# Kernel tuning notes

Hardware: AMD Instinct MI355X
Metric: run time of the kernel (lower is better)

The kernel has to match this reference:

```python
import jax, jax.numpy as jnp
import numpy as np

EMB = 1024
HEADS = 16
HEAD_DIM = EMB // HEADS
SEQ = 2048
BATCH = 2
FF = 4 * EMB


def gelu_tanh(x):
    # matches the hand-rolled GELU: 0.5*x*(1+tanh(sqrt(2/pi)*(x+0.044715*x^3)))
    c = jnp.sqrt(jnp.asarray(2.0 / jnp.pi, dtype=x.dtype))
    return 0.5 * x * (1.0 + jnp.tanh(c * (x + 0.044715 * x ** 3)))


def layernorm(x, scale, shift, eps=1e-5):
    mean = jnp.mean(x, axis=-1, keepdims=True)
    var = jnp.var(x, axis=-1, keepdims=True)  # unbiased=False
    return scale * (x - mean) * jax.lax.rsqrt(var + eps) + shift


def setup_inputs() -> dict:
    key = jax.random.key(0)
    ks = jax.random.split(key, 10)
    s = 1.0 / np.sqrt(EMB)
    sf = 1.0 / np.sqrt(FF)
    return {
        "x": jax.random.normal(ks[0], (BATCH, SEQ, EMB), jnp.float32),
        "Wq": jax.random.uniform(ks[1], (EMB, EMB), jnp.float32, -s, s),
        "Wk": jax.random.uniform(ks[2], (EMB, EMB), jnp.float32, -s, s),
        "Wv": jax.random.uniform(ks[3], (EMB, EMB), jnp.float32, -s, s),
        "Wo": jax.random.uniform(ks[4], (EMB, EMB), jnp.float32, -s, s),
        "bo": jnp.zeros((EMB,), jnp.float32),
        "ln1_g": jnp.ones((EMB,), jnp.float32),
        "ln1_b": jnp.zeros((EMB,), jnp.float32),
        "ln2_g": jnp.ones((EMB,), jnp.float32),
        "ln2_b": jnp.zeros((EMB,), jnp.float32),
        "W1": jax.random.uniform(ks[5], (EMB, FF), jnp.float32, -s, s),
        "b1": jnp.zeros((FF,), jnp.float32),
        "W2": jax.random.uniform(ks[6], (FF, EMB), jnp.float32, -sf, sf),
        "b2": jnp.zeros((EMB,), jnp.float32),
    }


def reference(x, Wq, Wk, Wv, Wo, bo, ln1_g, ln1_b, ln2_g, ln2_b, W1, b1, W2, b2):
    b, n, d = x.shape
    shortcut = x
    h = layernorm(x, ln1_g, ln1_b)
    # projections -> [b, heads, n, head_dim]
    def split_heads(t):
        return t.reshape(b, n, HEADS, HEAD_DIM).transpose(0, 2, 1, 3)
    q = split_heads(h @ Wq)
    k = split_heads(h @ Wk)
    v = split_heads(h @ Wv)
    scores = jnp.einsum("bhqd,bhkd->bhqk", q, k)
    causal = jnp.triu(jnp.ones((n, n), dtype=bool), k=1)
    scores = jnp.where(causal, -jnp.inf, scores)
    weights = jax.nn.softmax(scores / jnp.sqrt(jnp.asarray(HEAD_DIM, x.dtype)), axis=-1)
    ctx = jnp.einsum("bhqk,bhkd->bhqd", weights, v)
    ctx = ctx.transpose(0, 2, 1, 3).reshape(b, n, d)
    attn_out = ctx @ Wo + bo
    x = attn_out + shortcut
    shortcut = x
    h = layernorm(x, ln2_g, ln2_b)
    ff = gelu_tanh(h @ W1 + b1) @ W2 + b2
    return ff + shortcut
```

## Files before the change

kernel.cpp:

```cpp
#include <hip/hip_runtime.h>

typedef __bf16 bf16x8 __attribute__((ext_vector_type(8)));
typedef float f32x4 __attribute__((ext_vector_type(4)));
typedef unsigned short u16;

#define EMB 1024
#define SEQ 2048
#define BATCH 2
#define HEADS 16
#define HEAD_DIM 64
#define FF 4096
#define ROWS (BATCH * SEQ)

static __device__ __forceinline__ u16 f2bf(float f) {
    unsigned int u = __builtin_bit_cast(unsigned int, f);
    unsigned int r = (u + 0x7FFFu + ((u >> 16) & 1u)) >> 16;
    return (u16)r;
}

static __device__ __forceinline__ unsigned int pack_bf_trunc(float a, float b) {
    return __builtin_amdgcn_perm(__builtin_bit_cast(unsigned int, a),
                                 __builtin_bit_cast(unsigned int, b), 0x07060302u);
}

static __device__ __forceinline__ void gload16(const u16* g, u16* l) {
    __builtin_amdgcn_global_load_lds(
        (const __attribute__((address_space(1))) unsigned int*)(const void*)g,
        (__attribute__((address_space(3))) unsigned int*)(void*)l, 16, 0, 0);
}

__global__ __launch_bounds__(256) void transpose_f32_to_bf16(
    const float* __restrict__ in, u16* __restrict__ out, int R, int C) {
    __shared__ float tile[32][33];
    int c0 = blockIdx.x * 32, r0 = blockIdx.y * 32;
    int tx = threadIdx.x & 31, ty = threadIdx.x >> 5;
#pragma unroll
    for (int i = 0; i < 32; i += 8)
        tile[ty + i][tx] = in[(size_t)(r0 + ty + i) * C + c0 + tx];
    __syncthreads();
#pragma unroll
    for (int i = 0; i < 32; i += 8)
        out[(size_t)(c0 + ty + i) * R + r0 + tx] = f2bf(tile[tx][ty + i]);
}

__global__ __launch_bounds__(256) void transpose4_f32_to_bf16(
    const float* __restrict__ s0, const float* __restrict__ s1,
    const float* __restrict__ s2, const float* __restrict__ s3,
    u16* __restrict__ d0, u16* __restrict__ d1,
    u16* __restrict__ d2, u16* __restrict__ d3) {
    __shared__ float tile[32][33];
    const float* in;
    u16* out;
    switch (blockIdx.z) {
        case 0: in = s0; out = d0; break;
        case 1: in = s1; out = d1; break;
        case 2: in = s2; out = d2; break;
        default: in = s3; out = d3; break;
    }
    int c0 = blockIdx.x * 32, r0 = blockIdx.y * 32;
    int tx = threadIdx.x & 31, ty = threadIdx.x >> 5;
#pragma unroll
    for (int i = 0; i < 32; i += 8)
        tile[ty + i][tx] = in[(size_t)(r0 + ty + i) * EMB + c0 + tx];
    __syncthreads();
#pragma unroll
    for (int i = 0; i < 32; i += 8)
        out[(size_t)(c0 + ty + i) * EMB + r0 + tx] = f2bf(tile[tx][ty + i]);
}

__global__ __launch_bounds__(256) void ln_kernel(
    const float* __restrict__ x, const float* __restrict__ gamma,
    const float* __restrict__ beta, u16* __restrict__ out) {
    int row = blockIdx.x;
    int t = threadIdx.x;
    float4 v = reinterpret_cast<const float4*>(x + (size_t)row * EMB)[t];
    float s = v.x + v.y + v.z + v.w;
    float s2 = v.x * v.x + v.y * v.y + v.z * v.z + v.w * v.w;
#pragma unroll
    for (int off = 1; off < 64; off <<= 1) {
        s += __shfl_xor(s, off);
        s2 += __shfl_xor(s2, off);
    }
    __shared__ float sm[8];
    int wid = t >> 6;
    if ((t & 63) == 0) { sm[wid] = s; sm[wid + 4] = s2; }
    __syncthreads();
    s = sm[0] + sm[1] + sm[2] + sm[3];
    s2 = sm[4] + sm[5] + sm[6] + sm[7];
    float mean = s * (1.0f / EMB);
    float var = s2 * (1.0f / EMB) - mean * mean;
    float inv = rsqrtf(var + 1e-5f);
    float4 gv = reinterpret_cast<const float4*>(gamma)[t];
    float4 bv = reinterpret_cast<const float4*>(beta)[t];
    ushort4 o;
    o.x = f2bf((v.x - mean) * inv * gv.x + bv.x);
    o.y = f2bf((v.y - mean) * inv * gv.y + bv.y);
    o.z = f2bf((v.z - mean) * inv * gv.z + bv.z);
    o.w = f2bf((v.w - mean) * inv * gv.w + bv.w);
    reinterpret_cast<ushort4*>(out + (size_t)row * EMB)[t] = o;
}

template <int EPI, int BN>
__global__ __launch_bounds__(256) void gemm_bf16(
    const u16* __restrict__ A, const u16* __restrict__ B, void* __restrict__ Cout,
    const float* __restrict__ bias, const float* __restrict__ resid,
    void* __restrict__ Cout2, void* __restrict__ Cout3,
    int M, int N, int K) {
    __shared__ u16 As[128 * 64];
    __shared__ u16 Bs[BN * 64];
    constexpr int MI = (BN == 128) ? 4 : 2;
    constexpr int BSW = BN / 32;
    int tm = blockIdx.x * 128;
    int tn = blockIdx.y * BN;
    int t = threadIdx.x;
    int lane = t & 63, wid = t >> 6;
    int wr, wc;
    if constexpr (BN == 128) { wr = (wid >> 1) * 64; wc = (wid & 1) * 64; }
    else { wr = wid * 32; wc = 0; }
    int l15 = lane & 15, g = lane >> 4;
    const u16* Abase = A + (size_t)tm * K;
    const u16* Bbase = B + (size_t)tn * K;
    f32x4 acc[MI][4] = {};
    for (int k0 = 0; k0 < K; k0 += 64) {
        __syncthreads();
#pragma unroll
        for (int p = 0; p < 4; ++p) {
            int chunk = (wid * 4 + p) * 64 + lane;
            int row = chunk >> 3, c8 = (chunk & 7) * 8;
            gload16(Abase + (size_t)row * K + k0 + c8, &As[(wid * 4 + p) * 512]);
        }
#pragma unroll
        for (int p = 0; p < BSW; ++p) {
            int chunk = (wid * BSW + p) * 64 + lane;
            int row = chunk >> 3, c8 = (chunk & 7) * 8;
            gload16(Bbase + (size_t)row * K + k0 + c8, &Bs[(wid * BSW + p) * 512]);
        }
        __syncthreads();
#pragma unroll
        for (int kc = 0; kc < 2; ++kc) {
            int ko = kc * 32 + g * 8;
            bf16x8 af[MI], bfr[4];
#pragma unroll
            for (int i = 0; i < MI; ++i)
                af[i] = *reinterpret_cast<const bf16x8*>(&As[(wr + i * 16 + l15) * 64 + ko]);
#pragma unroll
            for (int j = 0; j < 4; ++j)
                bfr[j] = *reinterpret_cast<const bf16x8*>(&Bs[(wc + j * 16 + l15) * 64 + ko]);
#pragma unroll
            for (int i = 0; i < MI; ++i)
#pragma unroll
                for (int j = 0; j < 4; ++j)
                    acc[i][j] = __builtin_amdgcn_mfma_f32_16x16x32_bf16(af[i], bfr[j], acc[i][j], 0, 0, 0);
        }
    }
    int mb = tm + wr + g * 4;
    int nb = tn + wc + l15;
#pragma unroll
    for (int i = 0; i < MI; ++i) {
#pragma unroll
        for (int j = 0; j < 4; ++j) {
            int n = nb + j * 16;
#pragma unroll
            for (int r = 0; r < 4; ++r) {
                int m = mb + i * 16 + r;
                float val = acc[i][j][r];
                if constexpr (EPI == 0) {
                    ((u16*)Cout)[(size_t)m * N + n] = f2bf(val);
                } else if constexpr (EPI == 1) {
                    ((float*)Cout)[(size_t)m * N + n] =
                        val + bias[n] + resid[(size_t)m * N + n];
                } else if constexpr (EPI == 2) {
                    float xg = val + bias[n];
                    float x3 = xg + 0.044715f * xg * xg * xg;
                    float tz = 0.7978845608028654f * x3;
                    float th = 1.0f - 2.0f / (1.0f + __expf(2.0f * tz));
                    ((u16*)Cout)[(size_t)m * N + n] = f2bf(0.5f * xg * (1.0f + th));
                } else {
                    if (n < 1024) {
                        ((u16*)Cout)[(size_t)m * 1024 + n] = f2bf(val);
                    } else if (n < 2048) {
                        ((u16*)Cout2)[(size_t)m * 1024 + (n - 1024)] = f2bf(val);
                    } else {
                        int bb = m >> 11, ss = m & 2047;
                        ((u16*)Cout3)[((size_t)(bb * EMB + (n - 2048))) * SEQ + ss] = f2bf(val);
                    }
                }
            }
        }
    }
}

__global__ __launch_bounds__(64) void attn_kernel(
    const u16* __restrict__ Qb, const u16* __restrict__ Kb,
    const u16* __restrict__ Vt, u16* __restrict__ ctx) {
    __shared__ u16 P_lds[32][72];
    int bh = blockIdx.x;
    int b = bh >> 4, h = bh & 15;
    int qc = 63 - (int)blockIdx.y;
    int lane = threadIdx.x;
    int l15 = lane & 15, g = lane >> 4;
    int qbase = qc * 32;

    const u16* Qrow = Qb + (size_t)(b * SEQ) * EMB + h * 64;
    const u16* Krow = Kb + (size_t)(b * SEQ) * EMB + h * 64;
    const u16* Vrow = Vt + (size_t)(b * EMB + h * 64) * SEQ;

    bf16x8 qf[2][2];
#pragma unroll
    for (int qt = 0; qt < 2; ++qt)
#pragma unroll
        for (int kc = 0; kc < 2; ++kc) {
            bf16x8 v = *reinterpret_cast<const bf16x8*>(
                Qrow + (size_t)(qbase + qt * 16 + l15) * EMB + kc * 32 + g * 8);
            bf16x8 sv;
#pragma unroll
            for (int e = 0; e < 8; ++e) sv[e] = (__bf16)((float)v[e] * 0.125f);
            qf[qt][kc] = sv;
        }

    f32x4 ctx_acc[2][4] = {};
    float mrun[2] = {-1e30f, -1e30f};
    float lrun[2] = {0.f, 0.f};
    int nkt = qc / 2 + 1;

    bf16x8 kcur[8], knxt[8];
#pragma unroll
    for (int i = 0; i < 8; ++i) {
        int kc = i >> 2, ktile = i & 3;
        kcur[i] = *reinterpret_cast<const bf16x8*>(
            Krow + (size_t)(ktile * 16 + l15) * EMB + kc * 32 + g * 8);
    }

    for (int kt = 0; kt < nkt; ++kt) {
        int k0 = kt * 64;
        bool last = (kt == nkt - 1);
        bf16x8 vf[8];
#pragma unroll
        for (int i = 0; i < 8; ++i) {
            int kc = i >> 2, dt = i & 3;
            vf[i] = *reinterpret_cast<const bf16x8*>(
                Vrow + (size_t)(dt * 16 + l15) * SEQ + k0 + kc * 32 + g * 8);
        }
        f32x4 sacc[4][2] = {};
#pragma unroll
        for (int kc = 0; kc < 2; ++kc)
#pragma unroll
            for (int ktile = 0; ktile < 4; ++ktile)
#pragma unroll
                for (int qt = 0; qt < 2; ++qt)
                    sacc[ktile][qt] = __builtin_amdgcn_mfma_f32_16x16x32_bf16(
                        kcur[kc * 4 + ktile], qf[qt][kc], sacc[ktile][qt], 0, 0, 0);
        if (kt + 1 < nkt) {
#pragma unroll
            for (int i = 0; i < 8; ++i) {
                int kc = i >> 2, ktile = i & 3;
                knxt[i] = *reinterpret_cast<const bf16x8*>(
                    Krow + (size_t)(k0 + 64 + ktile * 16 + l15) * EMB + kc * 32 + g * 8);
            }
        }
#pragma unroll
        for (int qt = 0; qt < 2; ++qt) {
            float sv[16];
            float tmax = -1e30f;
            if (last) {
                int q = qbase + qt * 16 + l15;
#pragma unroll
                for (int ktile = 0; ktile < 4; ++ktile)
#pragma unroll
                    for (int r = 0; r < 4; ++r) {
                        int key = k0 + ktile * 16 + g * 4 + r;
                        float sx = (key > q) ? -1e30f : sacc[ktile][qt][r];
                        sv[ktile * 4 + r] = sx;
                        tmax = fmaxf(tmax, sx);
                    }
            } else {
#pragma unroll
                for (int ktile = 0; ktile < 4; ++ktile)
#pragma unroll
                    for (int r = 0; r < 4; ++r) {
                        float sx = sacc[ktile][qt][r];
                        sv[ktile * 4 + r] = sx;
                        tmax = fmaxf(tmax, sx);
                    }
            }
            tmax = fmaxf(tmax, __shfl_xor(tmax, 16));
            tmax = fmaxf(tmax, __shfl_xor(tmax, 32));
            if (!__all(tmax <= mrun[qt] + 8.0f)) {
                float mnew = fmaxf(mrun[qt], tmax);
                float corr = __expf(mrun[qt] - mnew);
                mrun[qt] = mnew;
                lrun[qt] *= corr;
                float corr4[4];
#pragma unroll
                for (int r = 0; r < 4; ++r) corr4[r] = __shfl(corr, g * 4 + r);
#pragma unroll
                for (int dt = 0; dt < 4; ++dt)
#pragma unroll
                    for (int r = 0; r < 4; ++r) ctx_acc[qt][dt][r] *= corr4[r];
            }
            float m = mrun[qt];
            float psum = 0.f;
#pragma unroll
            for (int idx = 0; idx < 16; ++idx) {
                float p = __expf(sv[idx] - m);
                sv[idx] = p;
                psum += p;
            }
            lrun[qt] += psum;
#pragma unroll
            for (int ktile = 0; ktile < 4; ++ktile) {
                uint2 w;
                w.x = pack_bf_trunc(sv[ktile * 4 + 1], sv[ktile * 4 + 0]);
                w.y = pack_bf_trunc(sv[ktile * 4 + 3], sv[ktile * 4 + 2]);
                *reinterpret_cast<uint2*>(&P_lds[qt * 16 + l15][ktile * 16 + g * 4]) = w;
            }
        }
        asm volatile("s_waitcnt lgkmcnt(0)" ::: "memory");
#pragma unroll
        for (int kc = 0; kc < 2; ++kc) {
            bf16x8 pf[2];
#pragma unroll
            for (int qt = 0; qt < 2; ++qt)
                pf[qt] = *reinterpret_cast<const bf16x8*>(&P_lds[qt * 16 + l15][kc * 32 + g * 8]);
#pragma unroll
            for (int dt = 0; dt < 4; ++dt)
#pragma unroll
                for (int qt = 0; qt < 2; ++qt)
                    ctx_acc[qt][dt] = __builtin_amdgcn_mfma_f32_16x16x32_bf16(
                        pf[qt], vf[kc * 4 + dt], ctx_acc[qt][dt], 0, 0, 0);
        }
#pragma unroll
        for (int i = 0; i < 8; ++i) kcur[i] = knxt[i];
    }
#pragma unroll
    for (int qt = 0; qt < 2; ++qt) {
        float lsum = lrun[qt];
        lsum += __shfl_xor(lsum, 16);
        lsum += __shfl_xor(lsum, 32);
        float d4[4];
#pragma unroll
        for (int r = 0; r < 4; ++r) d4[r] = __shfl(lsum, g * 4 + r);
#pragma unroll
        for (int dt = 0; dt < 4; ++dt)
#pragma unroll
            for (int r = 0; r < 4; ++r) {
                int q = qbase + qt * 16 + g * 4 + r;
                int d = h * 64 + dt * 16 + l15;
                ctx[(size_t)(b * SEQ + q) * EMB + d] = f2bf(ctx_acc[qt][dt][r] / d4[r]);
            }
    }
}

extern "C" void kernel_launch(void* const* d_in, const int* in_sizes, int n_in,
                              void* d_out, int out_size, void* d_ws, size_t ws_size,
                              hipStream_t stream) {
    const float* x    = (const float*)d_in[0];
    const float* Wq   = (const float*)d_in[1];
    const float* Wk   = (const float*)d_in[2];
    const float* Wv   = (const float*)d_in[3];
    const float* Wo   = (const float*)d_in[4];
    const float* bo   = (const float*)d_in[5];
    const float* ln1g = (const float*)d_in[6];
    const float* ln1b = (const float*)d_in[7];
    const float* ln2g = (const float*)d_in[8];
    const float* ln2b = (const float*)d_in[9];
    const float* W1   = (const float*)d_in[10];
    const float* b1   = (const float*)d_in[11];
    const float* W2   = (const float*)d_in[12];
    const float* b2   = (const float*)d_in[13];

    char* ws = (char*)d_ws;
    size_t off = 0;
    auto alloc = [&](size_t bytes) {
        void* p = ws + off;
        off += (bytes + 255) & ~(size_t)255;
        return p;
    };
    u16* h1     = (u16*)alloc((size_t)ROWS * EMB * 2);
    u16* Wqkvt  = (u16*)alloc((size_t)3 * EMB * EMB * 2);
    u16* Wot    = (u16*)alloc((size_t)EMB * EMB * 2);
    u16* W1t    = (u16*)alloc((size_t)FF * EMB * 2);
    u16* W2t    = (u16*)alloc((size_t)EMB * FF * 2);
    u16* Qb     = (u16*)alloc((size_t)ROWS * EMB * 2);
    u16* Kb     = (u16*)alloc((size_t)ROWS * EMB * 2);
    u16* Vtb    = (u16*)alloc((size_t)BATCH * EMB * SEQ * 2);
    u16* ctxb   = (u16*)alloc((size_t)ROWS * EMB * 2);
    float* x2   = (float*)alloc((size_t)ROWS * EMB * 4);
    u16* h2     = (u16*)alloc((size_t)ROWS * EMB * 2);
    u16* ff1    = (u16*)alloc((size_t)ROWS * FF * 2);

    u16* Wqt = Wqkvt;
    u16* Wkt = Wqkvt + (size_t)EMB * EMB;
    u16* Wvt = Wqkvt + (size_t)2 * EMB * EMB;

    transpose4_f32_to_bf16<<<dim3(32, 32, 4), 256, 0, stream>>>(
        Wq, Wk, Wv, Wo, Wqt, Wkt, Wvt, Wot);
    transpose_f32_to_bf16<<<dim3(128, 32), 256, 0, stream>>>(W1, W1t, EMB, FF);
    transpose_f32_to_bf16<<<dim3(32, 128), 256, 0, stream>>>(W2, W2t, FF, EMB);

    ln_kernel<<<ROWS, 256, 0, stream>>>(x, ln1g, ln1b, h1);

    gemm_bf16<4, 128><<<dim3(32, 24), 256, 0, stream>>>(h1, Wqkvt, Qb, nullptr, nullptr,
                                                        Kb, Vtb, ROWS, 3072, EMB);

    attn_kernel<<<dim3(32, 64), 64, 0, stream>>>(Qb, Kb, Vtb, ctxb);

    gemm_bf16<1, 64><<<dim3(32, 16), 256, 0, stream>>>(ctxb, Wot, x2, bo, x,
                                                       nullptr, nullptr, ROWS, EMB, EMB);

    ln_kernel<<<ROWS, 256, 0, stream>>>(x2, ln2g, ln2b, h2);

    gemm_bf16<2, 128><<<dim3(32, 32), 256, 0, stream>>>(h2, W1t, ff1, b1, nullptr,
                                                        nullptr, nullptr, ROWS, FF, EMB);
    gemm_bf16<1, 64><<<dim3(32, 16), 256, 0, stream>>>(ff1, W2t, (float*)d_out, b2, x2,
                                                       nullptr, nullptr, ROWS, EMB, FF);
}
```

Measured before the change: 415.2 us.

## Switch attention to 32x32x16 MFMA with register-resident P via permlane32 swap

Rewrites the attention kernel to use 32x32x16 bf16 MFMAs over one 32-query tile. The P matrix now stays in registers, rearranged with v_permlane32_swap instead of a round-trip through LDS. The softmax scale and log2(e) are folded into the Q projection epilogue so the kernel can use exp2 and skip per-load Q scaling. The K double-buffer is dropped and launch bounds request 2 waves per EU. This cuts LDS traffic, shuffles and instruction count, at the risk of higher register pressure and load latency no longer being hidden by the prefetch buffer.

```diff
diff --git a/kernel.cpp b/kernel.cpp
--- a/kernel.cpp
+++ b/kernel.cpp
@@ -2,6 +2,8 @@
 
 typedef __bf16 bf16x8 __attribute__((ext_vector_type(8)));
 typedef float f32x4 __attribute__((ext_vector_type(4)));
+typedef float f32x16 __attribute__((ext_vector_type(16)));
+typedef unsigned int u32x4 __attribute__((ext_vector_type(4)));
 typedef unsigned short u16;
 
 #define EMB 1024
@@ -11,6 +13,8 @@
 #define HEAD_DIM 64
 #define FF 4096
 #define ROWS (BATCH * SEQ)
+
+#define QSCALE 0.18033688011112042f
 
 static __device__ __forceinline__ u16 f2bf(float f) {
     unsigned int u = __builtin_bit_cast(unsigned int, f);
@@ -177,7 +181,7 @@
                     ((u16*)Cout)[(size_t)m * N + n] = f2bf(0.5f * xg * (1.0f + th));
                 } else {
                     if (n < 1024) {
-                        ((u16*)Cout)[(size_t)m * 1024 + n] = f2bf(val);
+                        ((u16*)Cout)[(size_t)m * 1024 + n] = f2bf(val * QSCALE);
                     } else if (n < 2048) {
                         ((u16*)Cout2)[(size_t)m * 1024 + (n - 1024)] = f2bf(val);
                     } else {
@@ -190,45 +194,38 @@
     }
 }
 
-__global__ __launch_bounds__(64) void attn_kernel(
+__global__ __launch_bounds__(64, 2) void attn_kernel(
     const u16* __restrict__ Qb, const u16* __restrict__ Kb,
     const u16* __restrict__ Vt, u16* __restrict__ ctx) {
-    __shared__ u16 P_lds[32][72];
     int bh = blockIdx.x;
     int b = bh >> 4, h = bh & 15;
     int qc = 63 - (int)blockIdx.y;
     int lane = threadIdx.x;
-    int l15 = lane & 15, g = lane >> 4;
+    int l31 = lane & 31, hi = lane >> 5;
+    int hi8 = hi * 8, hi4 = hi * 4;
     int qbase = qc * 32;
 
     const u16* Qrow = Qb + (size_t)(b * SEQ) * EMB + h * 64;
     const u16* Krow = Kb + (size_t)(b * SEQ) * EMB + h * 64;
     const u16* Vrow = Vt + (size_t)(b * EMB + h * 64) * SEQ;
 
-    bf16x8 qf[2][2];
-#pragma unroll
-    for (int qt = 0; qt < 2; ++qt)
-#pragma unroll
-        for (int kc = 0; kc < 2; ++kc) {
-            bf16x8 v = *reinterpret_cast<const bf16x8*>(
-                Qrow + (size_t)(qbase + qt * 16 + l15) * EMB + kc * 32 + g * 8);
-            bf16x8 sv;
-#pragma unroll
-            for (int e = 0; e < 8; ++e) sv[e] = (__bf16)((float)v[e] * 0.125f);
-            qf[qt][kc] = sv;
-        }
-
-    f32x4 ctx_acc[2][4] = {};
-    float mrun[2] = {-1e30f, -1e30f};
-    float lrun[2] = {0.f, 0.f};
+    bf16x8 qf[4];
+#pragma unroll
+    for (int kc = 0; kc < 4; ++kc)
+        qf[kc] = *reinterpret_cast<const bf16x8*>(
+            Qrow + (size_t)(qbase + l31) * EMB + kc * 16 + hi8);
+
+    f32x16 ctx_acc[2] = {};
+    float mrun = -1e30f;
+    float lrun = 0.f;
     int nkt = qc / 2 + 1;
 
-    bf16x8 kcur[8], knxt[8];
+    bf16x8 kcur[8];
 #pragma unroll
     for (int i = 0; i < 8; ++i) {
-        int kc = i >> 2, ktile = i & 3;
+        int kb = i >> 2, kc = i & 3;
         kcur[i] = *reinterpret_cast<const bf16x8*>(
-            Krow + (size_t)(ktile * 16 + l15) * EMB + kc * 32 + g * 8);
+            Krow + (size_t)(kb * 32 + l31) * EMB + kc * 16 + hi8);
     }
 
     for (int kt = 0; kt < nkt; ++kt) {
@@ -237,118 +234,106 @@
         bf16x8 vf[8];
 #pragma unroll
         for (int i = 0; i < 8; ++i) {
-            int kc = i >> 2, dt = i & 3;
+            int ks = i >> 1, dt = i & 1;
             vf[i] = *reinterpret_cast<const bf16x8*>(
-                Vrow + (size_t)(dt * 16 + l15) * SEQ + k0 + kc * 32 + g * 8);
-        }
-        f32x4 sacc[4][2] = {};
-#pragma unroll
-        for (int kc = 0; kc < 2; ++kc)
-#pragma unroll
-            for (int ktile = 0; ktile < 4; ++ktile)
-#pragma unroll
-                for (int qt = 0; qt < 2; ++qt)
-                    sacc[ktile][qt] = __builtin_amdgcn_mfma_f32_16x16x32_bf16(
-                        kcur[kc * 4 + ktile], qf[qt][kc], sacc[ktile][qt], 0, 0, 0);
+                Vrow + (size_t)(dt * 32 + l31) * SEQ + k0 + ks * 16 + hi8);
+        }
+        f32x16 sacc[2] = {};
+#pragma unroll
+        for (int kb = 0; kb < 2; ++kb)
+#pragma unroll
+            for (int kc = 0; kc < 4; ++kc)
+                sacc[kb] = __builtin_amdgcn_mfma_f32_32x32x16_bf16(
+                    kcur[kb * 4 + kc], qf[kc], sacc[kb], 0, 0, 0);
         if (kt + 1 < nkt) {
 #pragma unroll
             for (int i = 0; i < 8; ++i) {
-                int kc = i >> 2, ktile = i & 3;
-                knxt[i] = *reinterpret_cast<const bf16x8*>(
-                    Krow + (size_t)(k0 + 64 + ktile * 16 + l15) * EMB + kc * 32 + g * 8);
+                int kb = i >> 2, kc = i & 3;
+                kcur[i] = *reinterpret_cast<const bf16x8*>(
+                    Krow + (size_t)(k0 + 64 + kb * 32 + l31) * EMB + kc * 16 + hi8);
             }
         }
-#pragma unroll
-        for (int qt = 0; qt < 2; ++qt) {
-            float sv[16];
-            float tmax = -1e30f;
-            if (last) {
-                int q = qbase + qt * 16 + l15;
-#pragma unroll
-                for (int ktile = 0; ktile < 4; ++ktile)
-#pragma unroll
-                    for (int r = 0; r < 4; ++r) {
-                        int key = k0 + ktile * 16 + g * 4 + r;
-                        float sx = (key > q) ? -1e30f : sacc[ktile][qt][r];
-                        sv[ktile * 4 + r] = sx;
-                        tmax = fmaxf(tmax, sx);
-                    }
-            } else {
-#pragma unroll
-                for (int ktile = 0; ktile < 4; ++ktile)
-#pragma unroll
-                    for (int r = 0; r < 4; ++r) {
-                        float sx = sacc[ktile][qt][r];
-                        sv[ktile * 4 + r] = sx;
-                        tmax = fmaxf(tmax, sx);
-                    }
-            }
-            tmax = fmaxf(tmax, __shfl_xor(tmax, 16));
-            tmax = fmaxf(tmax, __shfl_xor(tmax, 32));
-            if (!__all(tmax <= mrun[qt] + 8.0f)) {
-                float mnew = fmaxf(mrun[qt], tmax);
-                float corr = __expf(mrun[qt] - mnew);
-                mrun[qt] = mnew;
-                lrun[qt] *= corr;
-                float corr4[4];
-#pragma unroll
-                for (int r = 0; r < 4; ++r) corr4[r] = __shfl(corr, g * 4 + r);
-#pragma unroll
-                for (int dt = 0; dt < 4; ++dt)
-#pragma unroll
-                    for (int r = 0; r < 4; ++r) ctx_acc[qt][dt][r] *= corr4[r];
-            }
-            float m = mrun[qt];
-            float psum = 0.f;
-#pragma unroll
-            for (int idx = 0; idx < 16; ++idx) {
-                float p = __expf(sv[idx] - m);
-                sv[idx] = p;
-                psum += p;
-            }
-            lrun[qt] += psum;
-#pragma unroll
-            for (int ktile = 0; ktile < 4; ++ktile) {
-                uint2 w;
-                w.x = pack_bf_trunc(sv[ktile * 4 + 1], sv[ktile * 4 + 0]);
-                w.y = pack_bf_trunc(sv[ktile * 4 + 3], sv[ktile * 4 + 2]);
-                *reinterpret_cast<uint2*>(&P_lds[qt * 16 + l15][ktile * 16 + g * 4]) = w;
-            }
-        }
-        asm volatile("s_waitcnt lgkmcnt(0)" ::: "memory");
-#pragma unroll
-        for (int kc = 0; kc < 2; ++kc) {
-            bf16x8 pf[2];
-#pragma unroll
-            for (int qt = 0; qt < 2; ++qt)
-                pf[qt] = *reinterpret_cast<const bf16x8*>(&P_lds[qt * 16 + l15][kc * 32 + g * 8]);
-#pragma unroll
-            for (int dt = 0; dt < 4; ++dt)
-#pragma unroll
-                for (int qt = 0; qt < 2; ++qt)
-                    ctx_acc[qt][dt] = __builtin_amdgcn_mfma_f32_16x16x32_bf16(
-                        pf[qt], vf[kc * 4 + dt], ctx_acc[qt][dt], 0, 0, 0);
-        }
-#pragma unroll
-        for (int i = 0; i < 8; ++i) kcur[i] = knxt[i];
-    }
-#pragma unroll
-    for (int qt = 0; qt < 2; ++qt) {
-        float lsum = lrun[qt];
-        lsum += __shfl_xor(lsum, 16);
-        lsum += __shfl_xor(lsum, 32);
-        float d4[4];
-#pragma unroll
-        for (int r = 0; r < 4; ++r) d4[r] = __shfl(lsum, g * 4 + r);
-#pragma unroll
-        for (int dt = 0; dt < 4; ++dt)
-#pragma unroll
-            for (int r = 0; r < 4; ++r) {
-                int q = qbase + qt * 16 + g * 4 + r;
-                int d = h * 64 + dt * 16 + l15;
-                ctx[(size_t)(b * SEQ + q) * EMB + d] = f2bf(ctx_acc[qt][dt][r] / d4[r]);
-            }
-    }
+        float sv[32];
+        float tmax = -1e30f;
+        if (last) {
+            int q = qbase + l31;
+#pragma unroll
+            for (int kb = 0; kb < 2; ++kb)
+#pragma unroll
+                for (int r = 0; r < 16; ++r) {
+                    int key = k0 + kb * 32 + (r & 3) + 8 * (r >> 2) + hi4;
+                    float sx = (key > q) ? -1e30f : sacc[kb][r];
+                    sv[kb * 16 + r] = sx;
+                    tmax = fmaxf(tmax, sx);
+                }
+        } else {
+#pragma unroll
+            for (int kb = 0; kb < 2; ++kb)
+#pragma unroll
+                for (int r = 0; r < 16; ++r) {
+                    float sx = sacc[kb][r];
+                    sv[kb * 16 + r] = sx;
+                    tmax = fmaxf(tmax, sx);
+                }
+        }
+        tmax = fmaxf(tmax, __shfl_xor(tmax, 32));
+        if (!__all(tmax <= mrun + 8.0f)) {
+            float mnew = fmaxf(mrun, tmax);
+            float corr = __builtin_amdgcn_exp2f(mrun - mnew);
+            mrun = mnew;
+            lrun *= corr;
+            float corr_r[16];
+#pragma unroll
+            for (int r = 0; r < 16; ++r)
+                corr_r[r] = __shfl(corr, (r & 3) + 8 * (r >> 2) + hi4);
+#pragma unroll
+            for (int dt = 0; dt < 2; ++dt)
+#pragma unroll
+                for (int r = 0; r < 16; ++r) ctx_acc[dt][r] *= corr_r[r];
+        }
+        float m = mrun;
+        float psum = 0.f;
+#pragma unroll
+        for (int i = 0; i < 32; ++i) {
+            float p = __builtin_amdgcn_exp2f(sv[i] - m);
+            sv[i] = p;
+            psum += p;
+        }
+        lrun += psum;
+        bf16x8 pa[4];
+#pragma unroll
+        for (int ks = 0; ks < 4; ++ks) {
+            int bse = (ks >> 1) * 16 + (ks & 1) * 8;
+            unsigned int w0 = pack_bf_trunc(sv[bse + 1], sv[bse + 0]);
+            unsigned int wA = pack_bf_trunc(sv[bse + 5], sv[bse + 4]);
+            unsigned int w1 = pack_bf_trunc(sv[bse + 3], sv[bse + 2]);
+            unsigned int wB = pack_bf_trunc(sv[bse + 7], sv[bse + 6]);
+            asm("v_permlane32_swap_b32 %0, %1" : "+v"(w0), "+v"(wA));
+            asm("v_permlane32_swap_b32 %0, %1" : "+v"(w1), "+v"(wB));
+            u32x4 words = {w0, w1, wA, wB};
+            pa[ks] = __builtin_bit_cast(bf16x8, words);
+        }
+#pragma unroll
+        for (int ks = 0; ks < 4; ++ks)
+#pragma unroll
+            for (int dt = 0; dt < 2; ++dt)
+                ctx_acc[dt] = __builtin_amdgcn_mfma_f32_32x32x16_bf16(
+                    pa[ks], vf[ks * 2 + dt], ctx_acc[dt], 0, 0, 0);
+    }
+    lrun += __shfl_xor(lrun, 32);
+    float linv = 1.0f / lrun;
+    float li[16];
+#pragma unroll
+    for (int r = 0; r < 16; ++r)
+        li[r] = __shfl(linv, (r & 3) + 8 * (r >> 2) + hi4);
+#pragma unroll
+    for (int dt = 0; dt < 2; ++dt)
+#pragma unroll
+        for (int r = 0; r < 16; ++r) {
+            int q = qbase + (r & 3) + 8 * (r >> 2) + hi4;
+            int d = h * 64 + dt * 32 + l31;
+            ctx[(size_t)(b * SEQ + q) * EMB + d] = f2bf(ctx_acc[dt][r] * li[r]);
+        }
 }
 
 extern "C" void kernel_launch(void* const* d_in, const int* in_sizes, int n_in,
```

Result: no change. 412.9 us (-0.5%).
